# Kernel tuning notes

Hardware: AMD Instinct MI355X
Metric: run time of the kernel (lower is better)

Reference implementation:

```python
import jax, jax.numpy as jnp
import numpy as np


def _lstm_dir(x, w_ih, w_hh, b, reverse):
    # x: [B,T,I]; w_ih: [4H,I]; w_hh: [4H,H]; b: [4H] (b_ih+b_hh combined)
    B = x.shape[0]
    H = w_hh.shape[1]
    pre = jnp.einsum('bti,gi->btg', x, w_ih) + b  # [B,T,4H]
    if reverse:
        pre = pre[:, ::-1]
    def step(carry, g):
        h, c = carry
        g = g + h @ w_hh.T
        i, f, gg, o = jnp.split(g, 4, axis=-1)  # torch gate order i,f,g,o
        i = jax.nn.sigmoid(i)
        f = jax.nn.sigmoid(f)
        gg = jnp.tanh(gg)
        o = jax.nn.sigmoid(o)
        c = f * c + i * gg
        h = o * jnp.tanh(c)
        return (h, c), h
    h0 = jnp.zeros((B, H), x.dtype)
    _, hs = jax.lax.scan(step, (h0, h0), pre.transpose(1, 0, 2))
    hs = hs.transpose(1, 0, 2)  # [B,T,H]
    if reverse:
        hs = hs[:, ::-1]
    return hs


def _bilstm_layer(x, w_ih, w_hh, b):
    # w_ih: [2,4H,I] (dir 0 = fwd, dir 1 = bwd)
    fwd = _lstm_dir(x, w_ih[0], w_hh[0], b[0], False)
    bwd = _lstm_dir(x, w_ih[1], w_hh[1], b[1], True)
    return jnp.concatenate([fwd, bwd], axis=-1)  # [B,T,2H]


def setup_inputs() -> dict:
    key = jax.random.key(0)
    V, E, H = 50000, 128, 128   # vocab, token embed dim, per-direction hidden
    B, S, T = 32, 50, 40        # batch, sentences, tokens per sentence
    D = 2 * H                   # 256 = bi-LSTM output width
    ks = iter(jax.random.split(key, 32))
    def p(shape, scale=0.05):
        return (jax.random.normal(next(ks), shape, dtype=jnp.float32) * scale)
    inp = {
        'inputs': jax.random.randint(next(ks), (B, S, T), 0, V, dtype=jnp.int32),
        'emb': p((V, E)),
        # sentence encoder LSTM (2 layers, bidirectional)
        'enc_w_ih0': p((2, 4 * H, E)), 'enc_w_hh0': p((2, 4 * H, H)), 'enc_b0': p((2, 4 * H)),
        'enc_w_ih1': p((2, 4 * H, D)), 'enc_w_hh1': p((2, 4 * H, H)), 'enc_b1': p((2, 4 * H)),
        # document LSTM (2 layers, bidirectional)
        'doc_w_ih0': p((2, 4 * H, D)), 'doc_w_hh0': p((2, 4 * H, H)), 'doc_b0': p((2, 4 * H)),
        'doc_w_ih1': p((2, 4 * H, D)), 'doc_w_hh1': p((2, 4 * H, H)), 'doc_b1': p((2, 4 * H)),
        # linear heads
        'content_w': p((1, D)), 'content_b': p((1,)),
        'docl_w': p((D, D)), 'docl_b': p((D,)),
        'sal_w': p((D, D)), 'sal_b': p((D,)),
        'nov_w': p((D, D)), 'nov_b': p((D,)),
    }
    return inp


def reference(inputs, emb,
              enc_w_ih0, enc_w_hh0, enc_b0, enc_w_ih1, enc_w_hh1, enc_b1,
              doc_w_ih0, doc_w_hh0, doc_b0, doc_w_ih1, doc_w_hh1, doc_b1,
              content_w, content_b, docl_w, docl_b, sal_w, sal_b, nov_w, nov_b):
    B, S, T = inputs.shape
    # --- sentence encoder over all B*S sentences ---
    tok = emb[inputs.reshape(-1, T)]                     # [B*S, T, E]
    h = _bilstm_layer(tok, enc_w_ih0, enc_w_hh0, enc_b0)  # [B*S, T, 2H]
    h = _bilstm_layer(h, enc_w_ih1, enc_w_hh1, enc_b1)
    sent = jnp.mean(h, axis=1).reshape(B, S, -1)         # [B, S, 256]
    # --- document LSTM over sentences ---
    out = _bilstm_layer(sent, doc_w_ih0, doc_w_hh0, doc_b0)
    out = _bilstm_layer(out, doc_w_ih1, doc_w_hh1, doc_b1)  # [B, S, 256]
    doc_emb = jnp.tanh(jnp.mean(out, axis=1) @ docl_w.T + docl_b)  # [B, 256]
    content = (out @ content_w.T + content_b)[..., 0]    # [B, S]
    sal_vec = doc_emb @ sal_w.T + sal_b                  # [B, 256]
    salience = jnp.einsum('bsd,bd->bs', out, sal_vec)    # [B, S]
    pred = content + salience
    # --- novelty recurrence over sentences ---
    summary0 = jnp.zeros((B, out.shape[2]), out.dtype)
    def step(summary, i):
        nov_vec = jnp.tanh(summary) @ nov_w.T + nov_b    # [B, 256]
        nov = jnp.einsum('bsd,bd->bs', out, nov_vec)     # [B, S]
        prob = jax.nn.sigmoid(pred - nov)
        summary = summary + prob[:, i, None] * out[:, i, :]
        return summary, nov
    _, novs = jax.lax.scan(step, summary0, jnp.arange(S))
    novelty = novs[-1]
    return pred - novelty
```

## Files before the change

kernel.cpp:

```cpp
#include <hip/hip_runtime.h>
#include <hip/hip_bf16.h>
#include <math.h>


__device__ __forceinline__ float sigm(float x) { return 1.f / (1.f + expf(-x)); }

__global__ void transpose_k(const float* __restrict__ in, float* __restrict__ out,
                            int R, int C) {
    __shared__ float tile[32][33];
    int z = blockIdx.z;
    in += (size_t)z * R * C;
    out += (size_t)z * R * C;
    int bx = blockIdx.x * 32, by = blockIdx.y * 32;
    int tx = threadIdx.x, ty = threadIdx.y;
    #pragma unroll
    for (int j = 0; j < 32; j += 8) {
        tile[ty + j][tx] = in[(size_t)(by + ty + j) * C + bx + tx];
    }
    __syncthreads();
    #pragma unroll
    for (int j = 0; j < 32; j += 8) {
        out[(size_t)(bx + ty + j) * R + by + tx] = tile[tx][ty + j];
    }
}

__global__ void pack_w(const float* __restrict__ ih, const float* __restrict__ hh,
                       float* __restrict__ dst, int E) {
    int ROWS = E + 128;
    size_t total = (size_t)2 * ROWS * 512;
    for (size_t i = (size_t)blockIdx.x * 256 + threadIdx.x; i < total;
         i += (size_t)gridDim.x * 256) {
        int g = (int)(i & 3);
        int k = (int)((i >> 2) & 127);
        size_t rr = i >> 9;
        int r = (int)(rr % ROWS);
        int dir = (int)(rr / ROWS);
        float v = (r < E) ? ih[((size_t)dir * 512 + g * 128 + k) * E + r]
                          : hh[((size_t)dir * 512 + g * 128 + k) * 128 + (r - E)];
        dst[i] = v;
    }
}

template <int E, int MODE>
__global__ __launch_bounds__(512) void word_scan2(
    const int* __restrict__ ids, const float* __restrict__ emb,
    const float* __restrict__ xin,
    const float* __restrict__ wpk,
    const float* __restrict__ bias,
    float* __restrict__ outp) {
    const int T = 40;
    const int ROWS = E + 128;
    int wg = blockIdx.x;
    int dir = wg / 100;
    int grp = wg - dir * 100;
    int base = grp * 16;
    int tid = threadIdx.x;
    int k = tid & 127;
    int gp = (tid >> 7) & 1;
    int hf = tid >> 8;
    int sb = hf * 8;

    __shared__ float xs[E][20];
    __shared__ float hs[128][20];
    __shared__ float pa[2][128][17];

    const float* wp = wpk + (size_t)dir * ROWS * 512 + k * 4 + gp * 2;
    const float* bb = bias + dir * 512;
    float bi = bb[k], bf_ = bb[128 + k], bg = bb[256 + k], bo = bb[384 + k];

    float c[8], ms[8];
    #pragma unroll
    for (int j = 0; j < 8; j++) { c[j] = 0.f; ms[j] = 0.f; }

    for (int t = 0; t < T; t++) {
        int te = dir ? (T - 1 - t) : t;
        {
            const int NF4 = 16 * (E / 4);
            for (int idx = tid; idx < NF4; idx += 512) {
                int s = idx / (E / 4);
                int e4 = idx - s * (E / 4);
                int seq = base + s;
                float4 v;
                if (MODE == 0) {
                    int id = ids[(size_t)seq * T + te];
                    v = *(const float4*)&emb[(size_t)id * 128 + e4 * 4];
                } else {
                    v = *(const float4*)&xin[((size_t)seq * T + te) * 256 + e4 * 4];
                }
                xs[e4 * 4 + 0][s] = v.x;
                xs[e4 * 4 + 1][s] = v.y;
                xs[e4 * 4 + 2][s] = v.z;
                xs[e4 * 4 + 3][s] = v.w;
            }
        }
        __syncthreads();

        float a0[8], a1[8];
        #pragma unroll
        for (int j = 0; j < 8; j++) { a0[j] = 0.f; a1[j] = 0.f; }

        #pragma unroll 4
        for (int e = 0; e < E; e++) {
            const float2 w = *(const float2*)(wp + (size_t)e * 512);
            const float4 x0 = *(const float4*)&xs[e][sb];
            const float4 x1 = *(const float4*)&xs[e][sb + 4];
            const float xv[8] = {x0.x, x0.y, x0.z, x0.w, x1.x, x1.y, x1.z, x1.w};
            #pragma unroll
            for (int j = 0; j < 8; j++) {
                a0[j] = fmaf(w.x, xv[j], a0[j]);
                a1[j] = fmaf(w.y, xv[j], a1[j]);
            }
        }
        if (t > 0) {
            const float* wh = wp + (size_t)E * 512;
            #pragma unroll 4
            for (int r = 0; r < 128; r++) {
                const float2 w = *(const float2*)(wh + (size_t)r * 512);
                const float4 x0 = *(const float4*)&hs[r][sb];
                const float4 x1 = *(const float4*)&hs[r][sb + 4];
                const float xv[8] = {x0.x, x0.y, x0.z, x0.w, x1.x, x1.y, x1.z, x1.w};
                #pragma unroll
                for (int j = 0; j < 8; j++) {
                    a0[j] = fmaf(w.x, xv[j], a0[j]);
                    a1[j] = fmaf(w.y, xv[j], a1[j]);
                }
            }
        }

        if (gp == 1) {
            #pragma unroll
            for (int j = 0; j < 8; j++) {
                pa[0][k][sb + j] = a0[j];
                pa[1][k][sb + j] = a1[j];
            }
        }
        __syncthreads();
        if (gp == 0) {
            float hv[8];
            #pragma unroll
            for (int j = 0; j < 8; j++) {
                float iv = sigm(a0[j] + bi);
                float fv = sigm(a1[j] + bf_);
                float gv = tanhf(pa[0][k][sb + j] + bg);
                float ov = sigm(pa[1][k][sb + j] + bo);
                c[j] = fv * c[j] + iv * gv;
                hv[j] = ov * tanhf(c[j]);
            }
            *(float4*)&hs[k][sb] = make_float4(hv[0], hv[1], hv[2], hv[3]);
            *(float4*)&hs[k][sb + 4] = make_float4(hv[4], hv[5], hv[6], hv[7]);
            if (MODE == 0) {
                #pragma unroll
                for (int j = 0; j < 8; j++) {
                    outp[(((size_t)(base + sb + j)) * T + te) * 256 +
                         (size_t)dir * 128 + k] = hv[j];
                }
            } else {
                #pragma unroll
                for (int j = 0; j < 8; j++) ms[j] += hv[j];
            }
        }
        __syncthreads();
    }
    if (MODE == 1 && gp == 0) {
        #pragma unroll
        for (int j = 0; j < 8; j++) {
            outp[(size_t)(base + sb + j) * 256 + (size_t)dir * 128 + k] =
                ms[j] * (1.f / T);
        }
    }
}

__global__ __launch_bounds__(256) void gemm_pre(
    const float* __restrict__ A, const float* __restrict__ Bt,
    const float* __restrict__ bias, float* __restrict__ C) {
    int dir = blockIdx.z;
    const float* B = Bt + (size_t)dir * 256 * 512;
    float* Cp = C + (size_t)dir * 1600 * 512;
    const float* bb = bias + (size_t)dir * 512;
    int n0 = blockIdx.x * 64, g0 = blockIdx.y * 64;
    int tid = threadIdx.x;
    int tx = tid & 15, ty = tid >> 4;
    __shared__ float AsT[32][72];
    __shared__ float Bs[32][72];
    float acc[4][4];
    #pragma unroll
    for (int i = 0; i < 4; i++)
        #pragma unroll
        for (int j = 0; j < 4; j++) acc[i][j] = 0.f;

    for (int k0 = 0; k0 < 256; k0 += 32) {
        #pragma unroll
        for (int it = 0; it < 2; it++) {
            int idx = tid + it * 256;
            int n = idx & 63, e4 = idx >> 6;
            float4 v = *(const float4*)&A[(size_t)(n0 + n) * 256 + k0 + e4 * 4];
            AsT[e4 * 4 + 0][n] = v.x;
            AsT[e4 * 4 + 1][n] = v.y;
            AsT[e4 * 4 + 2][n] = v.z;
            AsT[e4 * 4 + 3][n] = v.w;
        }
        #pragma unroll
        for (int it = 0; it < 2; it++) {
            int idx = tid + it * 256;
            int g4 = idx & 15, e = idx >> 4;
            float4 v = *(const float4*)&B[(size_t)(k0 + e) * 512 + g0 + g4 * 4];
            *(float4*)&Bs[e][g4 * 4] = v;
        }
        __syncthreads();
        #pragma unroll 8
        for (int kk = 0; kk < 32; kk++) {
            float4 a = *(const float4*)&AsT[kk][ty * 4];
            float4 b = *(const float4*)&Bs[kk][tx * 4];
            const float av[4] = {a.x, a.y, a.z, a.w};
            const float bv[4] = {b.x, b.y, b.z, b.w};
            #pragma unroll
            for (int i = 0; i < 4; i++)
                #pragma unroll
                for (int j = 0; j < 4; j++)
                    acc[i][j] = fmaf(av[i], bv[j], acc[i][j]);
        }
        __syncthreads();
    }
    #pragma unroll
    for (int i = 0; i < 4; i++) {
        #pragma unroll
        for (int j = 0; j < 4; j++) {
            Cp[(size_t)(n0 + ty * 4 + i) * 512 + g0 + tx * 4 + j] =
                acc[i][j] + bb[g0 + tx * 4 + j];
        }
    }
}

__global__ __launch_bounds__(512) void doc_scan2(
    const float* __restrict__ pre,
    const float* __restrict__ whh,
    float* __restrict__ outp) {
    const int S = 50;
    int wg = blockIdx.x;
    int dir = wg >> 4;
    int b0 = (wg & 15) * 2;
    int g = threadIdx.x;
    int k = g & 127, su = g >> 7;
    __shared__ float hsd[2][128];
    __shared__ float paD[2][512];
    const float* W = whh + (size_t)dir * 128 * 512;
    const float* p0 = pre + ((size_t)dir * 1600 + (size_t)b0 * 50) * 512;
    float cst = 0.f;
    for (int t = 0; t < S; t++) {
        int te = dir ? (S - 1 - t) : t;
        float a0 = p0[(size_t)te * 512 + g];
        float a1 = p0[((size_t)(50 + te)) * 512 + g];
        if (t > 0) {
            #pragma unroll 8
            for (int r = 0; r < 128; r++) {
                float w = W[(size_t)r * 512 + g];
                a0 = fmaf(w, hsd[0][r], a0);
                a1 = fmaf(w, hsd[1][r], a1);
            }
        }
        paD[0][g] = a0;
        paD[1][g] = a1;
        __syncthreads();
        if (g < 256) {
            float pi = paD[su][k], pf = paD[su][128 + k];
            float pg = paD[su][256 + k], po = paD[su][384 + k];
            float iv = sigm(pi), fv = sigm(pf), gv = tanhf(pg), ov = sigm(po);
            cst = fv * cst + iv * gv;
            float hv = ov * tanhf(cst);
            hsd[su][k] = hv;
            outp[((size_t)(b0 + su) * 50 + te) * 256 + (size_t)dir * 128 + k] = hv;
        }
        __syncthreads();
    }
}

__global__ __launch_bounds__(256) void head_kernel(
    const float* __restrict__ outv,
    const float* __restrict__ content_w,
    const float* __restrict__ content_b,
    const float* __restrict__ doclT,
    const float* __restrict__ docl_b,
    const float* __restrict__ salT,
    const float* __restrict__ sal_b,
    const float* __restrict__ novT,
    const float* __restrict__ nov_b,
    float* __restrict__ outp) {
    const int S = 50, D = 256;
    int b = blockIdx.x;
    int tid = threadIdx.x;
    __shared__ float oL[50][257];
    __shared__ float mb[256];
    __shared__ float de[256];
    __shared__ float svec[256];
    __shared__ float nvec[256];
    __shared__ float tsum[256];
    __shared__ float predL[64];
    __shared__ float nvL[64];
    __shared__ float red[4][64];

    const float* ob = outv + (size_t)b * S * D;
    for (int i = tid; i < S * D; i += 256) {
        int s = i >> 8, d = i & 255;
        oL[s][d] = ob[i];
    }
    __syncthreads();
    {
        float m = 0;
        for (int s = 0; s < S; s++) m += oL[s][tid];
        mb[tid] = m * (1.f / S);
    }
    __syncthreads();
    {
        float acc = docl_b[tid];
        for (int d = 0; d < D; d++) acc = fmaf(doclT[d * 256 + tid], mb[d], acc);
        de[tid] = tanhf(acc);
    }
    __syncthreads();
    {
        float acc = sal_b[tid];
        for (int d = 0; d < D; d++) acc = fmaf(salT[d * 256 + tid], de[d], acc);
        svec[tid] = acc;
    }
    __syncthreads();
    {
        int s = tid & 63, pw = tid >> 6;
        float ca = 0, sa = 0;
        if (s < S) {
            for (int i = 0; i < 64; i++) {
                int d = pw * 64 + i;
                float ov = oL[s][d];
                ca = fmaf(ov, content_w[d], ca);
                sa = fmaf(ov, svec[d], sa);
            }
        }
        red[pw][s] = ca + sa;
    }
    __syncthreads();
    if (tid < S) {
        predL[tid] = content_b[0] + red[0][tid] + red[1][tid] + red[2][tid] + red[3][tid];
    }
    float summ = 0.f;
    __syncthreads();
    for (int it = 0; it < S; ++it) {
        tsum[tid] = tanhf(summ);
        __syncthreads();
        {
            float acc = nov_b[tid];
            for (int d = 0; d < D; d++) acc = fmaf(novT[d * 256 + tid], tsum[d], acc);
            nvec[tid] = acc;
        }
        __syncthreads();
        {
            int s = tid & 63, pw = tid >> 6;
            float na = 0;
            if (s < S) {
                for (int i = 0; i < 64; i++) {
                    int d = pw * 64 + i;
                    na = fmaf(oL[s][d], nvec[d], na);
                }
            }
            red[pw][s] = na;
        }
        __syncthreads();
        if (tid < S) nvL[tid] = red[0][tid] + red[1][tid] + red[2][tid] + red[3][tid];
        __syncthreads();
        float prob = sigm(predL[it] - nvL[it]);
        summ = fmaf(prob, oL[it][tid], summ);
        __syncthreads();
    }
    if (tid < S) outp[(size_t)b * S + tid] = predL[tid] - nvL[tid];
}

extern "C" void kernel_launch(void* const* d_in, const int* in_sizes, int n_in,
                              void* d_out, int out_size, void* d_ws, size_t ws_size,
                              hipStream_t stream) {
    const int* ids = (const int*)d_in[0];
    const float* emb = (const float*)d_in[1];
    const float* e_ih0 = (const float*)d_in[2];
    const float* e_hh0 = (const float*)d_in[3];
    const float* e_b0 = (const float*)d_in[4];
    const float* e_ih1 = (const float*)d_in[5];
    const float* e_hh1 = (const float*)d_in[6];
    const float* e_b1 = (const float*)d_in[7];
    const float* d_ih0 = (const float*)d_in[8];
    const float* d_hh0 = (const float*)d_in[9];
    const float* d_b0 = (const float*)d_in[10];
    const float* d_ih1 = (const float*)d_in[11];
    const float* d_hh1 = (const float*)d_in[12];
    const float* d_b1 = (const float*)d_in[13];
    const float* content_w = (const float*)d_in[14];
    const float* content_b = (const float*)d_in[15];
    const float* docl_w = (const float*)d_in[16];
    const float* docl_b = (const float*)d_in[17];
    const float* sal_w = (const float*)d_in[18];
    const float* sal_b = (const float*)d_in[19];
    const float* nov_w = (const float*)d_in[20];
    const float* nov_b = (const float*)d_in[21];
    float* outp = (float*)d_out;

    float* ws = (float*)d_ws;
    size_t off = 0;
    auto alloc = [&](size_t n) { float* p = ws + off; off += n; return p; };
    float* wpk0 = alloc((size_t)2 * 256 * 512);
    float* wpk1 = alloc((size_t)2 * 384 * 512);
    float* bT_d0 = alloc((size_t)2 * 256 * 512);
    float* whh_d0 = alloc((size_t)2 * 128 * 512);
    float* bT_d1 = alloc((size_t)2 * 256 * 512);
    float* whh_d1 = alloc((size_t)2 * 128 * 512);
    float* wT_docl = alloc((size_t)256 * 256);
    float* wT_sal = alloc((size_t)256 * 256);
    float* wT_nov = alloc((size_t)256 * 256);
    float* h0out = alloc((size_t)1600 * 40 * 256);
    float* sent = alloc((size_t)1600 * 256);
    float* pre_d0 = alloc((size_t)2 * 1600 * 512);
    float* d0out = alloc((size_t)1600 * 256);
    float* pre_d1 = alloc((size_t)2 * 1600 * 512);
    float* dout = alloc((size_t)1600 * 256);
    (void)ws_size; (void)in_sizes; (void)n_in; (void)out_size;

    dim3 tb(32, 8);
    pack_w<<<1024, 256, 0, stream>>>(e_ih0, e_hh0, wpk0, 128);
    pack_w<<<1536, 256, 0, stream>>>(e_ih1, e_hh1, wpk1, 256);
    transpose_k<<<dim3(256 / 32, 512 / 32, 2), tb, 0, stream>>>(d_ih0, bT_d0, 512, 256);
    transpose_k<<<dim3(128 / 32, 512 / 32, 2), tb, 0, stream>>>(d_hh0, whh_d0, 512, 128);
    transpose_k<<<dim3(256 / 32, 512 / 32, 2), tb, 0, stream>>>(d_ih1, bT_d1, 512, 256);
    transpose_k<<<dim3(128 / 32, 512 / 32, 2), tb, 0, stream>>>(d_hh1, whh_d1, 512, 128);
    transpose_k<<<dim3(256 / 32, 256 / 32, 1), tb, 0, stream>>>(docl_w, wT_docl, 256, 256);
    transpose_k<<<dim3(256 / 32, 256 / 32, 1), tb, 0, stream>>>(sal_w, wT_sal, 256, 256);
    transpose_k<<<dim3(256 / 32, 256 / 32, 1), tb, 0, stream>>>(nov_w, wT_nov, 256, 256);

    word_scan2<128, 0><<<200, 512, 0, stream>>>(ids, emb, nullptr, wpk0, e_b0, h0out);
    word_scan2<256, 1><<<200, 512, 0, stream>>>(nullptr, nullptr, h0out, wpk1, e_b1, sent);

    gemm_pre<<<dim3(25, 8, 2), 256, 0, stream>>>(sent, bT_d0, d_b0, pre_d0);
    doc_scan2<<<32, 512, 0, stream>>>(pre_d0, whh_d0, d0out);
    gemm_pre<<<dim3(25, 8, 2), 256, 0, stream>>>(d0out, bT_d1, d_b1, pre_d1);
    doc_scan2<<<32, 512, 0, stream>>>(pre_d1, whh_d1, dout);

    head_kernel<<<32, 256, 0, stream>>>(dout, content_w, content_b, wT_docl, docl_b,
                                        wT_sal, sal_b, wT_nov, nov_b, outp);
}
```

Measured before the change: 2.508 ms.

## Hoist word-LSTM input projection into batched GEMM before recurrent scan

Result: no change. 2.501 ms (-0.3%).

```diff
diff --git a/kernel.cpp b/kernel.cpp
--- a/kernel.cpp
+++ b/kernel.cpp
@@ -38,6 +38,184 @@
         float v = (r < E) ? ih[((size_t)dir * 512 + g * 128 + k) * E + r]
                           : hh[((size_t)dir * 512 + g * 128 + k) * 128 + (r - E)];
         dst[i] = v;
+    }
+}
+
+__global__ void pack_bt(const float* __restrict__ ih, const float* __restrict__ b,
+                        float* __restrict__ bt, float* __restrict__ bv, int E) {
+    size_t total = (size_t)E * 1024;
+    for (size_t i = (size_t)blockIdx.x * 256 + threadIdx.x; i < total;
+         i += (size_t)gridDim.x * 256) {
+        int c = (int)(i & 1023);
+        int e = (int)(i >> 10);
+        int dir = c >> 9;
+        int gk = c & 511;
+        bt[i] = ih[((size_t)dir * 512 + gk) * E + e];
+        if (e == 0) bv[c] = b[dir * 512 + gk];
+    }
+}
+
+template <int K, int GATHER>
+__global__ __launch_bounds__(256, 4) void gemm_x(
+    const float* __restrict__ A, const int* __restrict__ ids,
+    const float* __restrict__ emb, const float* __restrict__ bt,
+    const float* __restrict__ bv, float* __restrict__ C) {
+    int n0 = blockIdx.x * 128;
+    int c0 = blockIdx.y * 128;
+    int tid = threadIdx.x;
+    int tx = tid & 15, ty = tid >> 4;
+    __shared__ float As[32][132];
+    __shared__ float Bs[32][132];
+    float acc[8][8];
+    #pragma unroll
+    for (int i = 0; i < 8; i++)
+        #pragma unroll
+        for (int j = 0; j < 8; j++) acc[i][j] = 0.f;
+
+    for (int k0 = 0; k0 < K; k0 += 32) {
+        #pragma unroll
+        for (int it = 0; it < 4; it++) {
+            int lin = tid + it * 256;
+            int r = lin >> 3, kq = lin & 7;
+            const float* src;
+            if (GATHER) {
+                src = emb + (size_t)ids[n0 + r] * 128;
+            } else {
+                src = A + (size_t)(n0 + r) * K;
+            }
+            float4 v = *(const float4*)&src[k0 + kq * 4];
+            As[kq * 4 + 0][r] = v.x;
+            As[kq * 4 + 1][r] = v.y;
+            As[kq * 4 + 2][r] = v.z;
+            As[kq * 4 + 3][r] = v.w;
+        }
+        #pragma unroll
+        for (int it = 0; it < 4; it++) {
+            int lin = tid + it * 256;
+            int kk = lin >> 5, c4 = lin & 31;
+            float4 v = *(const float4*)&bt[(size_t)(k0 + kk) * 1024 + c0 + c4 * 4];
+            *(float4*)&Bs[kk][c4 * 4] = v;
+        }
+        __syncthreads();
+        #pragma unroll 4
+        for (int kk = 0; kk < 32; kk++) {
+            float4 a0 = *(const float4*)&As[kk][ty * 8];
+            float4 a1 = *(const float4*)&As[kk][ty * 8 + 4];
+            float4 b0 = *(const float4*)&Bs[kk][tx * 8];
+            float4 b1 = *(const float4*)&Bs[kk][tx * 8 + 4];
+            const float av[8] = {a0.x, a0.y, a0.z, a0.w, a1.x, a1.y, a1.z, a1.w};
+            const float bvv[8] = {b0.x, b0.y, b0.z, b0.w, b1.x, b1.y, b1.z, b1.w};
+            #pragma unroll
+            for (int i = 0; i < 8; i++)
+                #pragma unroll
+                for (int j = 0; j < 8; j++)
+                    acc[i][j] = fmaf(av[i], bvv[j], acc[i][j]);
+        }
+        __syncthreads();
+    }
+    float bias8[8];
+    #pragma unroll
+    for (int j = 0; j < 8; j++) bias8[j] = bv[c0 + tx * 8 + j];
+    #pragma unroll
+    for (int i = 0; i < 8; i++) {
+        int row = n0 + ty * 8 + i;
+        float* cp = C + (size_t)row * 1024 + c0 + tx * 8;
+        float4 r0 = make_float4(acc[i][0] + bias8[0], acc[i][1] + bias8[1],
+                                acc[i][2] + bias8[2], acc[i][3] + bias8[3]);
+        float4 r1 = make_float4(acc[i][4] + bias8[4], acc[i][5] + bias8[5],
+                                acc[i][6] + bias8[6], acc[i][7] + bias8[7]);
+        *(float4*)cp = r0;
+        *(float4*)(cp + 4) = r1;
+    }
+}
+
+template <int MODE>
+__global__ __launch_bounds__(512) void word_scanH(
+    const float* __restrict__ pre,
+    const float* __restrict__ wph,
+    float* __restrict__ outp) {
+    const int T = 40;
+    int wg = blockIdx.x;
+    int dir = wg / 200;
+    int grp = wg - dir * 200;
+    int base = grp * 8;
+    int tid = threadIdx.x;
+    int k = tid & 127;
+    int gp = (tid >> 7) & 1;
+    int hf = tid >> 8;
+    int sb = hf * 4;
+
+    __shared__ float hs[128][12];
+    __shared__ float pa[2][128][12];
+
+    const float* wp = wph + (size_t)dir * 128 * 512 + k * 4 + gp * 2;
+
+    float c[4], ms[4];
+    #pragma unroll
+    for (int j = 0; j < 4; j++) { c[j] = 0.f; ms[j] = 0.f; }
+
+    for (int t = 0; t < T; t++) {
+        int te = dir ? (T - 1 - t) : t;
+        float a0[4], a1[4];
+        #pragma unroll
+        for (int j = 0; j < 4; j++) {
+            size_t n = (size_t)(base + sb + j) * T + te;
+            const float* pr = pre + n * 1024 + (size_t)dir * 512 + gp * 256 + k;
+            a0[j] = pr[0];
+            a1[j] = pr[128];
+        }
+        if (t > 0) {
+            #pragma unroll 8
+            for (int r = 0; r < 128; r++) {
+                const float2 w = *(const float2*)(wp + (size_t)r * 512);
+                const float4 x0 = *(const float4*)&hs[r][sb];
+                const float xv[4] = {x0.x, x0.y, x0.z, x0.w};
+                #pragma unroll
+                for (int j = 0; j < 4; j++) {
+                    a0[j] = fmaf(w.x, xv[j], a0[j]);
+                    a1[j] = fmaf(w.y, xv[j], a1[j]);
+                }
+            }
+        }
+        if (gp == 1) {
+            #pragma unroll
+            for (int j = 0; j < 4; j++) {
+                pa[0][k][sb + j] = a0[j];
+                pa[1][k][sb + j] = a1[j];
+            }
+        }
+        __syncthreads();
+        if (gp == 0) {
+            float hv[4];
+            #pragma unroll
+            for (int j = 0; j < 4; j++) {
+                float iv = sigm(a0[j]);
+                float fv = sigm(a1[j]);
+                float gv = tanhf(pa[0][k][sb + j]);
+                float ov = sigm(pa[1][k][sb + j]);
+                c[j] = fv * c[j] + iv * gv;
+                hv[j] = ov * tanhf(c[j]);
+            }
+            *(float4*)&hs[k][sb] = make_float4(hv[0], hv[1], hv[2], hv[3]);
+            if (MODE == 0) {
+                #pragma unroll
+                for (int j = 0; j < 4; j++) {
+                    outp[(((size_t)(base + sb + j)) * T + te) * 256 +
+                         (size_t)dir * 128 + k] = hv[j];
+                }
+            } else {
+                #pragma unroll
+                for (int j = 0; j < 4; j++) ms[j] += hv[j];
+            }
+        }
+        __syncthreads();
+    }
+    if (MODE == 1 && gp == 0) {
+        #pragma unroll
+        for (int j = 0; j < 4; j++) {
+            outp[(size_t)(base + sb + j) * 256 + (size_t)dir * 128 + k] =
+                ms[j] * (1.f / T);
+        }
     }
 }
 
@@ -275,16 +453,11 @@
 }
 
 __global__ __launch_bounds__(256) void head_kernel(
-    const float* __restrict__ outv,
-    const float* __restrict__ content_w,
-    const float* __restrict__ content_b,
-    const float* __restrict__ doclT,
-    const float* __restrict__ docl_b,
-    const float* __restrict__ salT,
-    const float* __restrict__ sal_b,
-    const float* __restrict__ novT,
-    const float* __restrict__ nov_b,
-    float* __restrict__ outp) {
+    const float* __restrict__ outv, const float* __restrict__ content_w,
+    const float* __restrict__ content_b, const float* __restrict__ doclT,
+    const float* __restrict__ docl_b, const float* __restrict__ salT,
+    const float* __restrict__ sal_b, const float* __restrict__ novT,
+    const float* __restrict__ nov_b, float* __restrict__ outp) {
     const int S = 50, D = 256;
     int b = blockIdx.x;
     int tid = threadIdx.x;
@@ -403,6 +576,12 @@
     auto alloc = [&](size_t n) { float* p = ws + off; off += n; return p; };
     float* wpk0 = alloc((size_t)2 * 256 * 512);
     float* wpk1 = alloc((size_t)2 * 384 * 512);
+    float* wph0 = alloc((size_t)2 * 128 * 512);
+    float* wph1 = alloc((size_t)2 * 128 * 512);
+    float* btw0 = alloc((size_t)128 * 1024);
+    float* btw1 = alloc((size_t)256 * 1024);
+    float* bv0 = alloc(1024);
+    float* bv1 = alloc(1024);
     float* bT_d0 = alloc((size_t)2 * 256 * 512);
     float* whh_d0 = alloc((size_t)2 * 128 * 512);
     float* bT_d1 = alloc((size_t)2 * 256 * 512);
@@ -410,17 +589,20 @@
     float* wT_docl = alloc((size_t)256 * 256);
     float* wT_sal = alloc((size_t)256 * 256);
     float* wT_nov = alloc((size_t)256 * 256);
-    float* h0out = alloc((size_t)1600 * 40 * 256);
     float* sent = alloc((size_t)1600 * 256);
     float* pre_d0 = alloc((size_t)2 * 1600 * 512);
     float* d0out = alloc((size_t)1600 * 256);
     float* pre_d1 = alloc((size_t)2 * 1600 * 512);
     float* dout = alloc((size_t)1600 * 256);
-    (void)ws_size; (void)in_sizes; (void)n_in; (void)out_size;
+    float* h0out = alloc((size_t)64000 * 256);
+    size_t need_fallback = off * 4;
+    float* pre = alloc((size_t)64000 * 1024);
+    size_t need_hoist = off * 4;
+    (void)in_sizes; (void)n_in; (void)out_size; (void)need_fallback;
+
+    bool hoist = ws_size >= need_hoist;
 
     dim3 tb(32, 8);
-    pack_w<<<1024, 256, 0, stream>>>(e_ih0, e_hh0, wpk0, 128);
-    pack_w<<<1536, 256, 0, stream>>>(e_ih1, e_hh1, wpk1, 256);
     transpose_k<<<dim3(256 / 32, 512 / 32, 2), tb, 0, stream>>>(d_ih0, bT_d0, 512, 256);
     transpose_k<<<dim3(128 / 32, 512 / 32, 2), tb, 0, stream>>>(d_hh0, whh_d0, 512, 128);
     transpose_k<<<dim3(256 / 32, 512 / 32, 2), tb, 0, stream>>>(d_ih1, bT_d1, 512, 256);
@@ -429,8 +611,25 @@
     transpose_k<<<dim3(256 / 32, 256 / 32, 1), tb, 0, stream>>>(sal_w, wT_sal, 256, 256);
     transpose_k<<<dim3(256 / 32, 256 / 32, 1), tb, 0, stream>>>(nov_w, wT_nov, 256, 256);
 
-    word_scan2<128, 0><<<200, 512, 0, stream>>>(ids, emb, nullptr, wpk0, e_b0, h0out);
-    word_scan2<256, 1><<<200, 512, 0, stream>>>(nullptr, nullptr, h0out, wpk1, e_b1, sent);
+    if (hoist) {
+        pack_w<<<256, 256, 0, stream>>>(e_hh0, e_hh0, wph0, 0);
+        pack_w<<<256, 256, 0, stream>>>(e_hh1, e_hh1, wph1, 0);
+        pack_bt<<<256, 256, 0, stream>>>(e_ih0, e_b0, btw0, bv0, 128);
+        pack_bt<<<512, 256, 0, stream>>>(e_ih1, e_b1, btw1, bv1, 256);
+
+        gemm_x<128, 1><<<dim3(500, 8), 256, 0, stream>>>(nullptr, ids, emb,
+                                                         btw0, bv0, pre);
+        word_scanH<0><<<400, 512, 0, stream>>>(pre, wph0, h0out);
+        gemm_x<256, 0><<<dim3(500, 8), 256, 0, stream>>>(h0out, nullptr, nullptr,
+                                                         btw1, bv1, pre);
+        word_scanH<1><<<400, 512, 0, stream>>>(pre, wph1, sent);
+    } else {
+        pack_w<<<1024, 256, 0, stream>>>(e_ih0, e_hh0, wpk0, 128);
+        pack_w<<<1536, 256, 0, stream>>>(e_ih1, e_hh1, wpk1, 256);
+        word_scan2<128, 0><<<200, 512, 0, stream>>>(ids, emb, nullptr, wpk0, e_b0, h0out);
+        word_scan2<256, 1><<<200, 512, 0, stream>>>(nullptr, nullptr, h0out, wpk1,
+                                                    e_b1, sent);
+    }
 
     gemm_pre<<<dim3(25, 8, 2), 256, 0, stream>>>(sent, bT_d0, d_b0, pre_d0);
     doc_scan2<<<32, 512, 0, stream>>>(pre_d0, whh_d0, d0out);
```
